# Kernel tuning notes

Measured on AMD Instinct MI355X. Metric: run time of the kernel, lower is better.

## Reference

```python
import jax, jax.numpy as jnp
import numpy as np
from jax import lax

B = 1024
LATENT = 512          # latent_dim (must equal conductor_output_dim, see forward feedback)
COND_H = 1024         # conductor_hidden_size
COND_OUT = 512        # conductor_output_dim
BOT_H = 1024          # bottom_decoder_hidden_size
OUT = 90              # output_size
NUM_SUB = 16          # hardcoded outer steps
SUB_LEN = 4           # hardcoded inner steps


def setup_inputs() -> dict:
    key = jax.random.key(0)
    ks = jax.random.split(key, 32)
    p = lambda k, shape: (jax.random.normal(k, shape, jnp.float32) * 0.02)
    bot_in = COND_OUT + OUT  # 602
    return {
        "z": jax.random.normal(ks[0], (B, LATENT), jnp.float32),
        "input_sequence": jax.random.uniform(ks[1], (B, NUM_SUB, SUB_LEN, OUT), jnp.float32),
        # fc_z
        "fc_z_w": p(ks[2], (COND_H, LATENT)), "fc_z_b": p(ks[3], (COND_H,)),
        # conductor LSTM (2 layers, torch gate order i,f,g,o)
        "cWih0": p(ks[4], (4 * COND_H, LATENT)), "cWhh0": p(ks[5], (4 * COND_H, COND_H)),
        "cbih0": p(ks[6], (4 * COND_H,)), "cbhh0": p(ks[7], (4 * COND_H,)),
        "cWih1": p(ks[8], (4 * COND_H, COND_H)), "cWhh1": p(ks[9], (4 * COND_H, COND_H)),
        "cbih1": p(ks[10], (4 * COND_H,)), "cbhh1": p(ks[11], (4 * COND_H,)),
        # fc_1 and conductor_fc
        "fc1_w": p(ks[12], (COND_OUT, COND_H)), "fc1_b": p(ks[13], (COND_OUT,)),
        "cfc_w": p(ks[14], (COND_OUT, COND_OUT)), "cfc_b": p(ks[15], (COND_OUT,)),
        # bottom decoder LSTM (2 layers)
        "bWih0": p(ks[16], (4 * BOT_H, bot_in)), "bWhh0": p(ks[17], (4 * BOT_H, BOT_H)),
        "bbih0": p(ks[18], (4 * BOT_H,)), "bbhh0": p(ks[19], (4 * BOT_H,)),
        "bWih1": p(ks[20], (4 * BOT_H, BOT_H)), "bWhh1": p(ks[21], (4 * BOT_H, BOT_H)),
        "bbih1": p(ks[22], (4 * BOT_H,)), "bbhh1": p(ks[23], (4 * BOT_H,)),
        # output layer
        "out_w": p(ks[24], (OUT, BOT_H)), "out_b": p(ks[25], (OUT,)),
    }


def _lstm_cell(x, h, c, Wih, Whh, bih, bhh):
    # torch LSTM cell: gates in i,f,g,o order
    gates = x @ Wih.T + bih + h @ Whh.T + bhh
    i, f, g, o = jnp.split(gates, 4, axis=-1)
    c_new = jax.nn.sigmoid(f) * c + jax.nn.sigmoid(i) * jnp.tanh(g)
    h_new = jax.nn.sigmoid(o) * jnp.tanh(c_new)
    return h_new, c_new


def reference(z, input_sequence, fc_z_w, fc_z_b,
              cWih0, cWhh0, cbih0, cbhh0, cWih1, cWhh1, cbih1, cbhh1,
              fc1_w, fc1_b, cfc_w, cfc_b,
              bWih0, bWhh0, bbih0, bbhh0, bWih1, bWhh1, bbih1, bbhh1,
              out_w, out_b):
    bsz = z.shape[0]
    out_dim = out_b.shape[0]
    bot_h = bWhh0.shape[1]

    # initial conductor state: tanh(fc_z(z)) used as (h, c) for both layers
    s0 = jnp.tanh(z @ fc_z_w.T + fc_z_b)  # [B, COND_H]
    cond_in0 = jnp.zeros((bsz, z.shape[1]), z.dtype)  # zeros(latent_dim)
    prev0 = jnp.zeros((bsz, out_dim), z.dtype)

    def outer(carry, _):
        cond_in, h1, c1, h2, c2, prev = carry
        h1, c1 = _lstm_cell(cond_in, h1, c1, cWih0, cWhh0, cbih0, cbhh0)
        h2, c2 = _lstm_cell(h1, h2, c2, cWih1, cWhh1, cbih1, cbhh1)
        cond_out = h2 @ fc1_w.T + fc1_b                    # [B, COND_OUT]
        emb = jnp.tanh(cond_out @ cfc_w.T + cfc_b)         # same every inner step
        z0 = jnp.zeros((bsz, bot_h), z.dtype)              # bottom state reset each subsequence

        def inner(ic, _):
            bh1, bc1, bh2, bc2, p = ic
            x = jnp.concatenate([emb, p], axis=1)          # [B, COND_OUT + OUT]
            bh1, bc1 = _lstm_cell(x, bh1, bc1, bWih0, bWhh0, bbih0, bbhh0)
            bh2, bc2 = _lstm_cell(bh1, bh2, bc2, bWih1, bWhh1, bbih1, bbhh1)
            p = bh2 @ out_w.T + out_b                      # [B, OUT]
            return (bh1, bc1, bh2, bc2, p), p

        (_, _, _, _, prev_last), ys = lax.scan(inner, (z0, z0, z0, z0, prev), None, length=SUB_LEN)
        # conductor_input for next step is fc_1 output (feedback in original code)
        return (cond_out, h1, c1, h2, c2, prev_last), ys   # ys: [SUB_LEN, B, OUT]

    _, outs = lax.scan(outer, (cond_in0, s0, s0, s0, s0, prev0), None, length=NUM_SUB)
    # outs: [NUM_SUB, SUB_LEN, B, OUT] -> [B, NUM_SUB*SUB_LEN, OUT]
    out = outs.reshape(NUM_SUB * SUB_LEN, bsz, out_dim).transpose(1, 0, 2)
    return jax.nn.sigmoid(out)
```

## Files before the change

kernel.cpp:

```cpp
#include <hip/hip_runtime.h>
#include <cstdint>
#include <cstddef>

typedef unsigned short u16;
typedef unsigned int u32;
typedef float f32x4 __attribute__((ext_vector_type(4)));
typedef _Float16 f16x8 __attribute__((ext_vector_type(8)));

__device__ __forceinline__ u16 f2h(float x) {
  _Float16 h = (_Float16)x;
  return __builtin_bit_cast(u16, h);
}
__device__ __forceinline__ float sigm(float x) { return 1.f / (1.f + __expf(-x)); }

__device__ __forceinline__ void gll16(const void* g, void* l) {
  __builtin_amdgcn_global_load_lds(
      (const __attribute__((address_space(1))) void*)g,
      (__attribute__((address_space(3))) void*)l, 16, 0, 0);
}

enum { M_PLAIN = 0, M_TANH = 1, M_OUT = 2 };

struct GemmP {
  const u16* A; int lda;
  const u16* W; int ldw;
  int K;
  const float* bias;
  int mode;
  int czero;
  u16* d0; int ld0;
  u16* d1; int ld1;
  float* c0;
  float* c1;
  float* fout;
};

template <bool CELL>
__global__ __launch_bounds__(512, 2) void gk(GemmP p) {
  __shared__ __align__(16) char sm[98304];
  const int tid = threadIdx.x;
  const int lane = tid & 63, wid = tid >> 6;
  const int wr = wid >> 1, wc = wid & 1;
  const int bRow = blockIdx.x * 128;
  const int nBase = blockIdx.y * (CELL ? 32 : 128);
  const int col0 = lane & 15, g4 = lane >> 4;

  f32x4 acc[2][4];
#pragma unroll
  for (int m = 0; m < 2; ++m)
#pragma unroll
    for (int n = 0; n < 4; ++n) acc[m][n] = f32x4{0.f, 0.f, 0.f, 0.f};

  const char* Ab = (const char*)p.A;
  const char* Wb = (const char*)p.W;
  const size_t ldaB = (size_t)p.lda * 2, ldwB = (size_t)p.ldw * 2;

  auto stage = [&](int buf, int kt) {
    char* base = sm + buf * 32768;
    const int kb = kt * 128;
#pragma unroll
    for (int i = 0; i < 2; ++i) {
      const int s = i * 512 + tid;
      const int row = s >> 3, ch = s & 7;
      const int sch = ch ^ (row & 7);
      gll16(Ab + (size_t)(bRow + row) * ldaB + (size_t)(kb + sch * 16),
            base + s * 16);
      const int wrow = CELL ? ((row >> 5) * 1024 + nBase + (row & 31)) : (nBase + row);
      gll16(Wb + (size_t)wrow * ldwB + (size_t)(kb + sch * 16),
            base + 16384 + s * 16);
    }
  };

  const int nt = p.K >> 6;
  stage(0, 0);
  stage(1, 1);
  int sb = 2, cb = 0;
  for (int t = 0; t < nt; ++t) {
    if (t + 2 < nt) {
      stage(sb, t + 2);
      sb = (sb == 2) ? 0 : sb + 1;
    }
    const int ahead = (nt - 1 - t < 2) ? (nt - 1 - t) : 2;
    if (ahead == 2)      asm volatile("s_waitcnt vmcnt(8)" ::: "memory");
    else if (ahead == 1) asm volatile("s_waitcnt vmcnt(4)" ::: "memory");
    else                 asm volatile("s_waitcnt vmcnt(0)" ::: "memory");
    __builtin_amdgcn_s_barrier();

    const char* Abase = sm + cb * 32768;
    const char* Wbase = Abase + 16384;
    f16x8 af[2][2], wf[2][4];
#pragma unroll
    for (int kf = 0; kf < 2; ++kf) {
      const int ch = kf * 4 + g4;
#pragma unroll
      for (int m = 0; m < 2; ++m) {
        const int r = wr * 32 + m * 16 + col0;
        af[kf][m] = *(const f16x8*)(Abase + r * 128 + ((ch ^ (r & 7)) << 4));
      }
#pragma unroll
      for (int n = 0; n < 4; ++n) {
        const int r = CELL ? (n * 32 + wc * 16 + col0) : (wc * 64 + n * 16 + col0);
        wf[kf][n] = *(const f16x8*)(Wbase + r * 128 + ((ch ^ (r & 7)) << 4));
      }
    }
#pragma unroll
    for (int kf = 0; kf < 2; ++kf)
#pragma unroll
      for (int m = 0; m < 2; ++m)
#pragma unroll
        for (int n = 0; n < 4; ++n)
          acc[m][n] = __builtin_amdgcn_mfma_f32_16x16x32_f16(af[kf][m], wf[kf][n],
                                                             acc[m][n], 0, 0, 0);
    asm volatile("s_waitcnt lgkmcnt(0)" ::: "memory");
    __builtin_amdgcn_s_barrier();
    cb = (cb == 2) ? 0 : cb + 1;
  }

  if (CELL) {
    const int j = nBase + wc * 16 + col0;
    const float bi = p.bias[j], bf_ = p.bias[j + 1024];
    const float bg = p.bias[j + 2048], bo = p.bias[j + 3072];
#pragma unroll
    for (int m = 0; m < 2; ++m) {
#pragma unroll
      for (int r = 0; r < 4; ++r) {
        const int b = bRow + wr * 32 + m * 16 + g4 * 4 + r;
        const float gi = acc[m][0][r] + bi;
        const float gf = acc[m][1][r] + bf_;
        const float gg = acc[m][2][r] + bg;
        const float go = acc[m][3][r] + bo;
        const size_t ci = (size_t)b * 1024 + j;
        const float cprev = p.czero ? 0.f : p.c0[ci];
        const float cn = sigm(gf) * cprev + sigm(gi) * tanhf(gg);
        p.c0[ci] = cn;
        const u16 hv = f2h(sigm(go) * tanhf(cn));
        p.d0[(size_t)b * p.ld0 + j] = hv;
        if (p.d1) p.d1[(size_t)b * p.ld1 + j] = hv;
      }
    }
  } else {
#pragma unroll
    for (int m = 0; m < 2; ++m)
#pragma unroll
      for (int n = 0; n < 4; ++n)
#pragma unroll
        for (int r = 0; r < 4; ++r) {
          const int b = bRow + wr * 32 + m * 16 + g4 * 4 + r;
          const int j = nBase + wc * 64 + n * 16 + col0;
          float v = acc[m][n][r] + p.bias[j];
          if (p.mode == M_TANH) {
            v = tanhf(v);
            const u16 hv = f2h(v);
            p.d0[(size_t)b * p.ld0 + j] = hv;
            if (p.d1) p.d1[(size_t)b * p.ld1 + j] = hv;
            if (p.c0) p.c0[(size_t)b * 1024 + j] = v;
            if (p.c1) p.c1[(size_t)b * 1024 + j] = v;
          } else if (p.mode == M_PLAIN) {
            p.d0[(size_t)b * p.ld0 + j] = f2h(v);
          } else {
            if (j < 90) {
              p.d0[(size_t)b * p.ld0 + j] = f2h(v);
              p.fout[(size_t)b * 5760 + j] = sigm(v);
            }
          }
        }
  }
}


__global__ void pack_w(u16* dst, const float* a, int Ka, const float* b, int Kb,
                       int gap, int Kp, int srcRows) {
  const int r = blockIdx.y;
  const int c = blockIdx.x * 256 + threadIdx.x;
  if (c >= Kp) return;
  float v = 0.f;
  if (r < srcRows) {
    if (c < Ka) v = a[(size_t)r * Ka + c];
    else if (c >= Ka + gap && c < Ka + gap + Kb) v = b[(size_t)r * Kb + (c - Ka - gap)];
  }
  dst[(size_t)r * Kp + c] = f2h(v);
}

struct BiasAll {
  float *bz, *bc0, *bc1, *bfc1, *bcfc, *bb0, *bb1, *bout;
  const float *fzb, *ci0, *ch0, *ci1, *ch1, *f1b, *cfb, *bi0, *bh0, *bi1, *bh1, *ob;
};
__global__ void pack_biases(BiasAll q) {
  int i = blockIdx.x * 256 + threadIdx.x;
  if (i < 1024) { q.bz[i] = q.fzb[i]; return; } i -= 1024;
  if (i < 4096) { q.bc0[i] = q.ci0[i] + q.ch0[i]; return; } i -= 4096;
  if (i < 4096) { q.bc1[i] = q.ci1[i] + q.ch1[i]; return; } i -= 4096;
  if (i < 512)  { q.bfc1[i] = q.f1b[i]; return; } i -= 512;
  if (i < 512)  { q.bcfc[i] = q.cfb[i]; return; } i -= 512;
  if (i < 4096) { q.bb0[i] = q.bi0[i] + q.bh0[i]; return; } i -= 4096;
  if (i < 4096) { q.bb1[i] = q.bi1[i] + q.bh1[i]; return; } i -= 4096;
  if (i < 128)  { q.bout[i] = (i < 90) ? q.ob[i] : 0.f; }
}

__global__ void conv_h(u16* dst, const float* src, long n) {
  for (long i = (long)blockIdx.x * blockDim.x + threadIdx.x; i < n;
       i += (long)gridDim.x * blockDim.x)
    dst[i] = f2h(src[i]);
}

__global__ void zero_init(u32* xc0, u32* xb0) {
  const int i = blockIdx.x * 256 + threadIdx.x;
  if (i < 1024 * 256) {
    xc0[(i >> 8) * 768 + (i & 255)] = 0;
  } else {
    const int k = i - 1024 * 256;
    xb0[(k >> 6) * 832 + 256 + (k & 63)] = 0;
  }
}

extern "C" void kernel_launch(void* const* d_in, const int* in_sizes, int n_in,
                              void* d_out, int out_size, void* d_ws, size_t ws_size,
                              hipStream_t stream) {
  const float* z      = (const float*)d_in[0];
  const float* fc_z_w = (const float*)d_in[2];
  const float* fc_z_b = (const float*)d_in[3];
  const float* cWih0  = (const float*)d_in[4];
  const float* cWhh0  = (const float*)d_in[5];
  const float* cbih0  = (const float*)d_in[6];
  const float* cbhh0  = (const float*)d_in[7];
  const float* cWih1  = (const float*)d_in[8];
  const float* cWhh1  = (const float*)d_in[9];
  const float* cbih1  = (const float*)d_in[10];
  const float* cbhh1  = (const float*)d_in[11];
  const float* fc1_w  = (const float*)d_in[12];
  const float* fc1_b  = (const float*)d_in[13];
  const float* cfc_w  = (const float*)d_in[14];
  const float* cfc_b  = (const float*)d_in[15];
  const float* bWih0  = (const float*)d_in[16];
  const float* bWhh0  = (const float*)d_in[17];
  const float* bbih0  = (const float*)d_in[18];
  const float* bbhh0  = (const float*)d_in[19];
  const float* bWih1  = (const float*)d_in[20];
  const float* bWhh1  = (const float*)d_in[21];
  const float* bbih1  = (const float*)d_in[22];
  const float* bbhh1  = (const float*)d_in[23];
  const float* out_w  = (const float*)d_in[24];
  const float* out_b  = (const float*)d_in[25];
  float* outp = (float*)d_out;

  char* w = (char*)d_ws;
  auto alloc = [&](size_t bytes) {
    char* p = w;
    w += (bytes + 255) & ~(size_t)255;
    return p;
  };
  u16* Wz   = (u16*)alloc((size_t)1024 * 512 * 2);
  u16* Wc0  = (u16*)alloc((size_t)4096 * 1536 * 2);
  u16* Wc1  = (u16*)alloc((size_t)4096 * 2048 * 2);
  u16* Wb0  = (u16*)alloc((size_t)4096 * 1664 * 2);
  u16* Wb1  = (u16*)alloc((size_t)4096 * 2048 * 2);
  u16* Wfc1 = (u16*)alloc((size_t)512 * 1024 * 2);
  u16* Wcfc = (u16*)alloc((size_t)512 * 512 * 2);
  u16* Wout = (u16*)alloc((size_t)128 * 1024 * 2);
  u16* zh   = (u16*)alloc((size_t)1024 * 512 * 2);
  u16* Xc0  = (u16*)alloc((size_t)1024 * 1536 * 2);
  u16* Xc1  = (u16*)alloc((size_t)1024 * 2048 * 2);
  u16* Xb0  = (u16*)alloc((size_t)1024 * 1664 * 2);
  u16* Xb1  = (u16*)alloc((size_t)1024 * 2048 * 2);
  float* cc0  = (float*)alloc((size_t)1024 * 1024 * 4);
  float* cc1  = (float*)alloc((size_t)1024 * 1024 * 4);
  float* cbb0 = (float*)alloc((size_t)1024 * 1024 * 4);
  float* cbb1 = (float*)alloc((size_t)1024 * 1024 * 4);
  float* bz   = (float*)alloc(1024 * 4);
  float* bc0  = (float*)alloc(4096 * 4);
  float* bc1  = (float*)alloc(4096 * 4);
  float* bfc1 = (float*)alloc(512 * 4);
  float* bcfc = (float*)alloc(512 * 4);
  float* bb0  = (float*)alloc(4096 * 4);
  float* bb1  = (float*)alloc(4096 * 4);
  float* bout = (float*)alloc(128 * 4);

  const dim3 blk(256), blk5(512);

  pack_w<<<dim3(2, 1024), blk, 0, stream>>>(Wz,   fc_z_w, 512,  nullptr, 0,    0,  512,  1024);
  pack_w<<<dim3(6, 4096), blk, 0, stream>>>(Wc0,  cWih0,  512,  cWhh0,   1024, 0,  1536, 4096);
  pack_w<<<dim3(8, 4096), blk, 0, stream>>>(Wc1,  cWih1,  1024, cWhh1,   1024, 0,  2048, 4096);
  pack_w<<<dim3(7, 4096), blk, 0, stream>>>(Wb0,  bWih0,  602,  bWhh0,   1024, 38, 1664, 4096);
  pack_w<<<dim3(8, 4096), blk, 0, stream>>>(Wb1,  bWih1,  1024, bWhh1,   1024, 0,  2048, 4096);
  pack_w<<<dim3(4, 512),  blk, 0, stream>>>(Wfc1, fc1_w,  1024, nullptr, 0,    0,  1024, 512);
  pack_w<<<dim3(2, 512),  blk, 0, stream>>>(Wcfc, cfc_w,  512,  nullptr, 0,    0,  512,  512);
  pack_w<<<dim3(4, 128),  blk, 0, stream>>>(Wout, out_w,  1024, nullptr, 0,    0,  1024, 90);
  {
    BiasAll q{bz, bc0, bc1, bfc1, bcfc, bb0, bb1, bout,
              fc_z_b, cbih0, cbhh0, cbih1, cbhh1, fc1_b, cfc_b,
              bbih0, bbhh0, bbih1, bbhh1, out_b};
    pack_biases<<<dim3(80), blk, 0, stream>>>(q);
  }
  conv_h<<<dim3(512), blk, 0, stream>>>(zh, z, 1024L * 512);
  zero_init<<<dim3(1280), blk, 0, stream>>>((u32*)Xc0, (u32*)Xb0);

  {
    GemmP p;
    p.A = zh; p.lda = 512; p.W = Wz; p.ldw = 512; p.K = 512; p.bias = bz;
    p.mode = M_TANH; p.czero = 0;
    p.d0 = Xc0 + 512; p.ld0 = 1536; p.d1 = Xc1 + 1024; p.ld1 = 2048;
    p.c0 = cc0; p.c1 = cc1; p.fout = nullptr;
    gk<false><<<dim3(8, 8), blk5, 0, stream>>>(p);
  }

  for (int t = 0; t < 16; ++t) {
    {
      GemmP p;
      p.A = Xc0; p.lda = 1536; p.W = Wc0; p.ldw = 1536; p.K = 1536; p.bias = bc0;
      p.mode = 0; p.czero = 0;
      p.d0 = Xc0 + 512; p.ld0 = 1536; p.d1 = Xc1; p.ld1 = 2048;
      p.c0 = cc0; p.c1 = nullptr; p.fout = nullptr;
      gk<true><<<dim3(8, 32), blk5, 0, stream>>>(p);
    }
    {
      GemmP p;
      p.A = Xc1; p.lda = 2048; p.W = Wc1; p.ldw = 2048; p.K = 2048; p.bias = bc1;
      p.mode = 0; p.czero = 0;
      p.d0 = Xc1 + 1024; p.ld0 = 2048; p.d1 = nullptr; p.ld1 = 0;
      p.c0 = cc1; p.c1 = nullptr; p.fout = nullptr;
      gk<true><<<dim3(8, 32), blk5, 0, stream>>>(p);
    }
    {
      GemmP p;
      p.A = Xc1 + 1024; p.lda = 2048; p.W = Wfc1; p.ldw = 1024; p.K = 1024;
      p.bias = bfc1; p.mode = M_PLAIN; p.czero = 0;
      p.d0 = Xc0; p.ld0 = 1536; p.d1 = nullptr; p.ld1 = 0;
      p.c0 = nullptr; p.c1 = nullptr; p.fout = nullptr;
      gk<false><<<dim3(8, 4), blk5, 0, stream>>>(p);
    }
    {
      GemmP p;
      p.A = Xc0; p.lda = 1536; p.W = Wcfc; p.ldw = 512; p.K = 512;
      p.bias = bcfc; p.mode = M_TANH; p.czero = 0;
      p.d0 = Xb0; p.ld0 = 1664; p.d1 = nullptr; p.ld1 = 0;
      p.c0 = nullptr; p.c1 = nullptr; p.fout = nullptr;
      gk<false><<<dim3(8, 4), blk5, 0, stream>>>(p);
    }
    for (int s = 0; s < 4; ++s) {
      {
        GemmP p;
        p.A = Xb0; p.lda = 1664; p.W = Wb0; p.ldw = 1664;
        p.K = (s == 0) ? 640 : 1664; p.bias = bb0;
        p.mode = 0; p.czero = (s == 0);
        p.d0 = Xb0 + 640; p.ld0 = 1664; p.d1 = Xb1; p.ld1 = 2048;
        p.c0 = cbb0; p.c1 = nullptr; p.fout = nullptr;
        gk<true><<<dim3(8, 32), blk5, 0, stream>>>(p);
      }
      {
        GemmP p;
        p.A = Xb1; p.lda = 2048; p.W = Wb1; p.ldw = 2048;
        p.K = (s == 0) ? 1024 : 2048; p.bias = bb1;
        p.mode = 0; p.czero = (s == 0);
        p.d0 = Xb1 + 1024; p.ld0 = 2048; p.d1 = nullptr; p.ld1 = 0;
        p.c0 = cbb1; p.c1 = nullptr; p.fout = nullptr;
        gk<true><<<dim3(8, 32), blk5, 0, stream>>>(p);
      }
      {
        GemmP p;
        p.A = Xb1 + 1024; p.lda = 2048; p.W = Wout; p.ldw = 1024; p.K = 1024;
        p.bias = bout; p.mode = M_OUT; p.czero = 0;
        p.d0 = Xb0 + 512; p.ld0 = 1664; p.d1 = nullptr; p.ld1 = 0;
        p.c0 = nullptr; p.c1 = nullptr;
        p.fout = outp + (size_t)(t * 4 + s) * 90;
        gk<false><<<dim3(8, 1), blk5, 0, stream>>>(p);
      }
    }
  }
}
```

Measured before the change: 5.248 ms.

## Use 4-deep LDS ring to drop trailing barrier and remap cell blocks per XCD

The K-loop staging ring grows from three to four 32KB LDS buffers. With prefetch distance two, the buffer being refilled can no longer be one another wave is still reading, so the end-of-iteration lgkmcnt wait and second barrier are removed. This halves the barrier count per tile. The LSTM cell GEMM launches also switch to a 1D grid of 256 blocks, remapped so each XCD (block id mod 8) handles a contiguous group of 4 column tiles across all 8 row tiles, which should improve L2 reuse of the weight and activation tiles. The LDS footprint rises to 128KB per block, which limits how many blocks can share a CU.

```diff
diff --git a/kernel.cpp b/kernel.cpp
--- a/kernel.cpp
+++ b/kernel.cpp
@@ -37,12 +37,22 @@
 
 template <bool CELL>
 __global__ __launch_bounds__(512, 2) void gk(GemmP p) {
-  __shared__ __align__(16) char sm[98304];
+  __shared__ __align__(16) char sm[131072];
   const int tid = threadIdx.x;
   const int lane = tid & 63, wid = tid >> 6;
   const int wr = wid >> 1, wc = wid & 1;
-  const int bRow = blockIdx.x * 128;
-  const int nBase = blockIdx.y * (CELL ? 32 : 128);
+  int bx, by;
+  if (CELL) {
+    const int hw = blockIdx.x;
+    const int xcd = hw & 7, idx = hw >> 3;
+    by = xcd * 4 + (idx >> 3);
+    bx = idx & 7;
+  } else {
+    bx = blockIdx.x;
+    by = blockIdx.y;
+  }
+  const int bRow = bx * 128;
+  const int nBase = by * (CELL ? 32 : 128);
   const int col0 = lane & 15, g4 = lane >> 4;
 
   f32x4 acc[2][4];
@@ -74,19 +84,15 @@
   const int nt = p.K >> 6;
   stage(0, 0);
   stage(1, 1);
-  int sb = 2, cb = 0;
   for (int t = 0; t < nt; ++t) {
-    if (t + 2 < nt) {
-      stage(sb, t + 2);
-      sb = (sb == 2) ? 0 : sb + 1;
-    }
+    if (t + 2 < nt) stage((t + 2) & 3, t + 2);
     const int ahead = (nt - 1 - t < 2) ? (nt - 1 - t) : 2;
     if (ahead == 2)      asm volatile("s_waitcnt vmcnt(8)" ::: "memory");
     else if (ahead == 1) asm volatile("s_waitcnt vmcnt(4)" ::: "memory");
     else                 asm volatile("s_waitcnt vmcnt(0)" ::: "memory");
     __builtin_amdgcn_s_barrier();
 
-    const char* Abase = sm + cb * 32768;
+    const char* Abase = sm + (t & 3) * 32768;
     const char* Wbase = Abase + 16384;
     f16x8 af[2][2], wf[2][4];
 #pragma unroll
@@ -111,9 +117,6 @@
         for (int n = 0; n < 4; ++n)
           acc[m][n] = __builtin_amdgcn_mfma_f32_16x16x32_f16(af[kf][m], wf[kf][n],
                                                              acc[m][n], 0, 0, 0);
-    asm volatile("s_waitcnt lgkmcnt(0)" ::: "memory");
-    __builtin_amdgcn_s_barrier();
-    cb = (cb == 2) ? 0 : cb + 1;
   }
 
   if (CELL) {
@@ -276,6 +279,7 @@
   float* bout = (float*)alloc(128 * 4);
 
   const dim3 blk(256), blk5(512);
+  const dim3 gcell(256);
 
   pack_w<<<dim3(2, 1024), blk, 0, stream>>>(Wz,   fc_z_w, 512,  nullptr, 0,    0,  512,  1024);
   pack_w<<<dim3(6, 4096), blk, 0, stream>>>(Wc0,  cWih0,  512,  cWhh0,   1024, 0,  1536, 4096);
@@ -310,7 +314,7 @@
       p.mode = 0; p.czero = 0;
       p.d0 = Xc0 + 512; p.ld0 = 1536; p.d1 = Xc1; p.ld1 = 2048;
       p.c0 = cc0; p.c1 = nullptr; p.fout = nullptr;
-      gk<true><<<dim3(8, 32), blk5, 0, stream>>>(p);
+      gk<true><<<gcell, blk5, 0, stream>>>(p);
     }
     {
       GemmP p;
@@ -318,7 +322,7 @@
       p.mode = 0; p.czero = 0;
       p.d0 = Xc1 + 1024; p.ld0 = 2048; p.d1 = nullptr; p.ld1 = 0;
       p.c0 = cc1; p.c1 = nullptr; p.fout = nullptr;
-      gk<true><<<dim3(8, 32), blk5, 0, stream>>>(p);
+      gk<true><<<gcell, blk5, 0, stream>>>(p);
     }
     {
       GemmP p;
@@ -344,7 +348,7 @@
         p.mode = 0; p.czero = (s == 0);
         p.d0 = Xb0 + 640; p.ld0 = 1664; p.d1 = Xb1; p.ld1 = 2048;
         p.c0 = cbb0; p.c1 = nullptr; p.fout = nullptr;
-        gk<true><<<dim3(8, 32), blk5, 0, stream>>>(p);
+        gk<true><<<gcell, blk5, 0, stream>>>(p);
       }
       {
         GemmP p;
@@ -353,7 +357,7 @@
         p.mode = 0; p.czero = (s == 0);
         p.d0 = Xb1 + 1024; p.ld0 = 2048; p.d1 = nullptr; p.ld1 = 0;
         p.c0 = cbb1; p.c1 = nullptr; p.fout = nullptr;
-        gk<true><<<dim3(8, 32), blk5, 0, stream>>>(p);
+        gk<true><<<gcell, blk5, 0, stream>>>(p);
       }
       {
         GemmP p;
```

Result: faster. 5.003 ms (-4.7%).
